# Performance work log

Measured on AMD Instinct MI355X. Metric: run time of the kernel, lower is better.

## Reference

```python
import jax, jax.numpy as jnp
import numpy as np

TWO_PI = 2.0 * 3.14159  # matches the torch source constant exactly
N_RINGS = 5
N_ORIENT = 8


def setup_inputs() -> dict:
    key = jax.random.key(0)
    k1, k2, k3 = jax.random.split(key, 3)
    B, N, CIN, COUT = 4, 32768, 32, 32
    features = jax.random.normal(k1, (B, N, CIN), dtype=jnp.float32)
    # radial in [0,1), angular in [0, 2*pi)
    coords01 = jax.random.uniform(k2, (B, N, 2), dtype=jnp.float32)
    geodesic_coords = coords01 * jnp.array([1.0, TWO_PI], dtype=jnp.float32)
    filters = jax.random.normal(k3, (N_RINGS, N_ORIENT, CIN, COUT), dtype=jnp.float32) * 0.01
    bias = jnp.zeros((COUT,), dtype=jnp.float32)
    return {"features": features, "geodesic_coords": geodesic_coords,
            "filters": filters, "bias": bias}


def reference(features, geodesic_coords, filters, bias):
    radial = geodesic_coords[:, :, 0]
    angular = geodesic_coords[:, :, 1]
    # torch .long() truncates toward zero; values are non-negative so astype matches
    ring_idx = jnp.clip((radial * N_RINGS).astype(jnp.int32), 0, N_RINGS - 1)
    orient_idx = jnp.clip((angular * N_ORIENT / TWO_PI).astype(jnp.int32), 0, N_ORIENT - 1)
    # gather per-point filter matrix: (B, N, Cin, Cout)
    W = filters[ring_idx, orient_idx]
    out = jnp.einsum('bnc,bncd->bnd', features, W) + bias
    return out
```

## Files before the change

kernel.cpp:

```cpp
#include <hip/hip_runtime.h>


#define NPTS_PER_BLOCK 64
#define THREADS 256

__global__ __launch_bounds__(THREADS, 4)
void geodesic_conv_kernel(const float* __restrict__ feat,
                          const float* __restrict__ coords,
                          const float* __restrict__ filt,
                          const float* __restrict__ bias,
                          float* __restrict__ out)
{
    __shared__ float4 lds_f4[NPTS_PER_BLOCK * 8];
    __shared__ int    lds_bin[NPTS_PER_BLOCK];

    const int tid   = threadIdx.x;
    const int pbase = blockIdx.x * NPTS_PER_BLOCK;

    const float4* gf4 = reinterpret_cast<const float4*>(feat) + (size_t)pbase * 8;
    lds_f4[tid]       = gf4[tid];
    lds_f4[tid + 256] = gf4[tid + 256];

    if (tid < NPTS_PER_BLOCK) {
        float2 rc = reinterpret_cast<const float2*>(coords)[pbase + tid];
        int ri = (int)(rc.x * 5.0f);
        ri = min(max(ri, 0), 4);
        const float TWO_PI_F = (float)(2.0 * 3.14159);
        int oi = (int)((rc.y * 8.0f) / TWO_PI_F);
        oi = min(max(oi, 0), 7);
        lds_bin[tid] = ri * 8 + oi;
    }
    __syncthreads();

    const int wave = tid >> 6;
    const int lane = tid & 63;
    const int half = lane >> 5;
    const int d    = lane & 31;
    const float bs = bias[d];

    for (int i = 0; i < 8; ++i) {
        const int p   = wave * 16 + i * 2 + half;
        const int bin = lds_bin[p];
        const float* W = filt + (size_t)bin * 1024 + d;
        float acc = 0.0f;
        #pragma unroll
        for (int c4 = 0; c4 < 8; ++c4) {
            float4 fv = lds_f4[p * 8 + c4];
            acc += fv.x * W[(c4 * 4 + 0) * 32];
            acc += fv.y * W[(c4 * 4 + 1) * 32];
            acc += fv.z * W[(c4 * 4 + 2) * 32];
            acc += fv.w * W[(c4 * 4 + 3) * 32];
        }
        out[(size_t)(pbase + p) * 32 + d] = acc + bs;
    }
}

extern "C" void kernel_launch(void* const* d_in, const int* in_sizes, int n_in,
                              void* d_out, int out_size, void* d_ws, size_t ws_size,
                              hipStream_t stream) {
    const float* feat   = (const float*)d_in[0];
    const float* coords = (const float*)d_in[1];
    const float* filt   = (const float*)d_in[2];
    const float* bias   = (const float*)d_in[3];
    float* out = (float*)d_out;

    const int npts    = in_sizes[0] / 32;
    const int nblocks = npts / NPTS_PER_BLOCK;
    geodesic_conv_kernel<<<nblocks, THREADS, 0, stream>>>(feat, coords, filt, bias, out);
}
```

Before: 88.55 us.

## Sort points by filter bin, then compute per-point matvec with wave-uniform weights

Adds histogram, scan and scatter kernels that counting-sort points by their (ring, orientation) bin, then runs a compute kernel where each thread owns one point, holds its 32 features in registers and loops over the distinct bins present in its wave, reading those filter weights as wave-uniform loads. The aim is to avoid the scattered per-lane weight gathers and turn weight reads into broadcast or scalar loads. In exchange it adds three extra launches, workspace traffic and a gathered feature read per thread. It also uses 64+ accumulator registers per thread, and waves that still hold several bins repeat the full 32x32 loop once per bin. The pk encoding assumes npts < 2^20, and the scan assumes at most 128 histogram blocks.

```diff
diff --git a/kernel.cpp b/kernel.cpp
--- a/kernel.cpp
+++ b/kernel.cpp
@@ -1,70 +1,136 @@
 #include <hip/hip_runtime.h>
 
 
-#define NPTS_PER_BLOCK 64
-#define THREADS 256
+#define NBINS 40
+#define K1_THREADS 1024
+#define MAX_NBLK 128
 
-__global__ __launch_bounds__(THREADS, 4)
-void geodesic_conv_kernel(const float* __restrict__ feat,
-                          const float* __restrict__ coords,
-                          const float* __restrict__ filt,
-                          const float* __restrict__ bias,
-                          float* __restrict__ out)
-{
-    __shared__ float4 lds_f4[NPTS_PER_BLOCK * 8];
-    __shared__ int    lds_bin[NPTS_PER_BLOCK];
+__device__ __forceinline__ int bin_of(float2 rc) {
+    const float TWO_PI_F = (float)(2.0 * 3.14159);
+    int ri = (int)(rc.x * 5.0f);
+    ri = min(max(ri, 0), 4);
+    int oi = (int)((rc.y * 8.0f) / TWO_PI_F);
+    oi = min(max(oi, 0), 7);
+    return ri * 8 + oi;
+}
 
-    const int tid   = threadIdx.x;
-    const int pbase = blockIdx.x * NPTS_PER_BLOCK;
+__global__ __launch_bounds__(K1_THREADS)
+void k_hist(const float2* __restrict__ coords, int* __restrict__ hist, int npts) {
+    __shared__ int h[NBINS];
+    const int tid = threadIdx.x;
+    if (tid < NBINS) h[tid] = 0;
+    __syncthreads();
+    const int p = blockIdx.x * K1_THREADS + tid;
+    if (p < npts) atomicAdd(&h[bin_of(coords[p])], 1);
+    __syncthreads();
+    if (tid < NBINS) hist[blockIdx.x * NBINS + tid] = h[tid];
+}
 
-    const float4* gf4 = reinterpret_cast<const float4*>(feat) + (size_t)pbase * 8;
-    lds_f4[tid]       = gf4[tid];
-    lds_f4[tid + 256] = gf4[tid + 256];
-
-    if (tid < NPTS_PER_BLOCK) {
-        float2 rc = reinterpret_cast<const float2*>(coords)[pbase + tid];
-        int ri = (int)(rc.x * 5.0f);
-        ri = min(max(ri, 0), 4);
-        const float TWO_PI_F = (float)(2.0 * 3.14159);
-        int oi = (int)((rc.y * 8.0f) / TWO_PI_F);
-        oi = min(max(oi, 0), 7);
-        lds_bin[tid] = ri * 8 + oi;
+__global__ __launch_bounds__(K1_THREADS)
+void k_scan(const int* __restrict__ hist, int* __restrict__ blkoff, int nblk) {
+    __shared__ int lh[MAX_NBLK * NBINS];
+    __shared__ int base[NBINS];
+    const int tid = threadIdx.x;
+    for (int i = tid; i < nblk * NBINS; i += K1_THREADS) lh[i] = hist[i];
+    __syncthreads();
+    if (tid < NBINS) {
+        int s = 0;
+        for (int k = 0; k < nblk; ++k) { int v = lh[k * NBINS + tid]; lh[k * NBINS + tid] = s; s += v; }
+        base[tid] = s;
     }
     __syncthreads();
+    if (tid == 0) {
+        int s = 0;
+        for (int b = 0; b < NBINS; ++b) { int v = base[b]; base[b] = s; s += v; }
+    }
+    __syncthreads();
+    if (tid < NBINS) for (int k = 0; k < nblk; ++k) lh[k * NBINS + tid] += base[tid];
+    __syncthreads();
+    for (int i = tid; i < nblk * NBINS; i += K1_THREADS) blkoff[i] = lh[i];
+}
 
+__global__ __launch_bounds__(K1_THREADS)
+void k_scatter(const float2* __restrict__ coords, const int* __restrict__ blkoff,
+               int* __restrict__ sorted_pk, int npts) {
+    __shared__ int off[NBINS];
+    __shared__ int cnt[NBINS];
+    const int tid = threadIdx.x;
+    if (tid < NBINS) { off[tid] = blkoff[blockIdx.x * NBINS + tid]; cnt[tid] = 0; }
+    __syncthreads();
+    const int p = blockIdx.x * K1_THREADS + tid;
+    if (p < npts) {
+        const int b = bin_of(coords[p]);
+        const int r = atomicAdd(&cnt[b], 1);
+        sorted_pk[off[b] + r] = p | (b << 20);
+    }
+}
+
+__global__ __launch_bounds__(256)
+void k_gemm(const float* __restrict__ feat, const float* __restrict__ filt,
+            const float* __restrict__ bias, const int* __restrict__ sorted_pk,
+            float* __restrict__ out, int npts) {
+    const int tid  = threadIdx.x;
     const int wave = tid >> 6;
     const int lane = tid & 63;
-    const int half = lane >> 5;
-    const int d    = lane & 31;
-    const float bs = bias[d];
+    const int pos  = (blockIdx.x * 4 + wave) * 64 + lane;
 
-    for (int i = 0; i < 8; ++i) {
-        const int p   = wave * 16 + i * 2 + half;
-        const int bin = lds_bin[p];
-        const float* W = filt + (size_t)bin * 1024 + d;
-        float acc = 0.0f;
+    const int pk  = sorted_pk[pos];
+    const int idx = pk & 0xFFFFF;
+    const int b   = pk >> 20;
+
+    const float4* fp = reinterpret_cast<const float4*>(feat + (size_t)idx * 32);
+    float f[32];
+    #pragma unroll
+    for (int g = 0; g < 8; ++g) {
+        float4 v = fp[g];
+        f[g * 4 + 0] = v.x; f[g * 4 + 1] = v.y; f[g * 4 + 2] = v.z; f[g * 4 + 3] = v.w;
+    }
+
+    float acc[32];
+    #pragma unroll
+    for (int d = 0; d < 32; ++d) acc[d] = bias[d];
+
+    unsigned long long rem = __ballot(1);
+    while (rem) {
+        const int src = (int)__ffsll((long long)rem) - 1;
+        const int bb  = __shfl(b, src);
+        const unsigned long long m = __ballot(b == bb);
+        rem &= ~m;
+        const bool act = (b == bb);
+        const float* __restrict__ W = filt + (size_t)bb * 1024;
         #pragma unroll
-        for (int c4 = 0; c4 < 8; ++c4) {
-            float4 fv = lds_f4[p * 8 + c4];
-            acc += fv.x * W[(c4 * 4 + 0) * 32];
-            acc += fv.y * W[(c4 * 4 + 1) * 32];
-            acc += fv.z * W[(c4 * 4 + 2) * 32];
-            acc += fv.w * W[(c4 * 4 + 3) * 32];
+        for (int c = 0; c < 32; ++c) {
+            const float fc = act ? f[c] : 0.0f;
+            #pragma unroll
+            for (int d = 0; d < 32; ++d)
+                acc[d] = fmaf(fc, W[c * 32 + d], acc[d]);
         }
-        out[(size_t)(pbase + p) * 32 + d] = acc + bs;
     }
+
+    float4* op = reinterpret_cast<float4*>(out + (size_t)idx * 32);
+    #pragma unroll
+    for (int g = 0; g < 8; ++g)
+        op[g] = make_float4(acc[g * 4 + 0], acc[g * 4 + 1], acc[g * 4 + 2], acc[g * 4 + 3]);
 }
 
 extern "C" void kernel_launch(void* const* d_in, const int* in_sizes, int n_in,
                               void* d_out, int out_size, void* d_ws, size_t ws_size,
                               hipStream_t stream) {
-    const float* feat   = (const float*)d_in[0];
-    const float* coords = (const float*)d_in[1];
-    const float* filt   = (const float*)d_in[2];
-    const float* bias   = (const float*)d_in[3];
+    const float*  feat   = (const float*)d_in[0];
+    const float2* coords = (const float2*)d_in[1];
+    const float*  filt   = (const float*)d_in[2];
+    const float*  bias   = (const float*)d_in[3];
     float* out = (float*)d_out;
 
-    const int npts    = in_sizes[0] / 32;
-    const int nblocks = npts / NPTS_PER_BLOCK;
-    geodesic_conv_kernel<<<nblocks, THREADS, 0, stream>>>(feat, coords, filt, bias, out);
+    const int npts = in_sizes[0] / 32;
+    const int nblk = (npts + K1_THREADS - 1) / K1_THREADS;
+
+    int* sorted_pk = (int*)d_ws;
+    int* hist      = sorted_pk + npts;
+    int* blkoff    = hist + nblk * NBINS;
+
+    k_hist   <<<nblk, K1_THREADS, 0, stream>>>(coords, hist, npts);
+    k_scan   <<<1,    K1_THREADS, 0, stream>>>(hist, blkoff, nblk);
+    k_scatter<<<nblk, K1_THREADS, 0, stream>>>(coords, blkoff, sorted_pk, npts);
+    k_gemm   <<<npts / 256, 256,  0, stream>>>(feat, filt, bias, sorted_pk, out, npts);
 }
```

After: 120.9 us. 1.36x slower.
